# Optimization experiments

Hardware: AMD Instinct MI355X
Metric: run time of the kernel (lower is better)

## Reference

```python
import jax, jax.numpy as jnp
import numpy as np

IN_CH, HID, H1, H2, C2, OUT = 13, 64, 4, 2, 32, 1
NEG_SLOPE = 0.2  # PyG GATConv leaky_relu slope
BN_EPS = 1e-5


def _gat_layer(x, src, dst, N, W, att_src, att_dst, bias, heads, ch, concat):
    # x: [N, F_in]; W: [F_in, heads*ch]; att_*: [heads, ch]
    h = (x @ W).reshape(N, heads, ch)                      # [N,H,C]
    a_src = jnp.sum(h * att_src, axis=-1)                  # [N,H]
    a_dst = jnp.sum(h * att_dst, axis=-1)                  # [N,H]
    alpha = jax.nn.leaky_relu(a_src[src] + a_dst[dst], NEG_SLOPE)  # [E,H]
    # segment softmax over incoming edges of each dst node
    amax = jax.ops.segment_max(alpha, dst, num_segments=N)         # [N,H]
    e = jnp.exp(alpha - amax[dst])
    denom = jax.ops.segment_sum(e, dst, num_segments=N)
    alpha = e / denom[dst]                                 # [E,H]
    msg = h[src] * alpha[:, :, None]                       # [E,H,C]
    out = jax.ops.segment_sum(msg, dst, num_segments=N)    # [N,H,C]
    if concat:
        return out.reshape(N, heads * ch) + bias
    return out.mean(axis=1) + bias


def _with_self_loops(edge_index, N):
    loop = jnp.arange(N, dtype=edge_index.dtype)
    src = jnp.concatenate([edge_index[0], loop])
    dst = jnp.concatenate([edge_index[1], loop])
    return src, dst


def setup_inputs() -> dict:
    key = jax.random.key(0)
    ks = jax.random.split(key, 12)
    N, E = 50000, 800000
    glorot = lambda k, shp: jax.random.normal(k, shp, jnp.float32) * np.sqrt(2.0 / (shp[0] + shp[-1]))
    return {
        "x": jax.random.normal(ks[0], (N, IN_CH), jnp.float32),
        "edge_index": jax.random.randint(ks[1], (2, E), 0, N, dtype=jnp.int64 if jax.config.jax_enable_x64 else jnp.int32),
        "W1": glorot(ks[2], (IN_CH, H1 * HID)),
        "att_src1": glorot(ks[3], (H1, HID)),
        "att_dst1": glorot(ks[4], (H1, HID)),
        "b1": jnp.zeros((H1 * HID,), jnp.float32),
        "gamma1": jnp.ones((H1 * HID,), jnp.float32),
        "beta1": jnp.zeros((H1 * HID,), jnp.float32),
        "W2": glorot(ks[5], (H1 * HID, H2 * C2)),
        "att_src2": glorot(ks[6], (H2, C2)),
        "att_dst2": glorot(ks[7], (H2, C2)),
        "b2": jnp.zeros((C2,), jnp.float32),
        "Wc": glorot(ks[8], (C2, OUT)),
        "bc": jnp.zeros((OUT,), jnp.float32),
    }


def reference(x, edge_index, W1, att_src1, att_dst1, b1, gamma1, beta1,
              W2, att_src2, att_dst2, b2, Wc, bc):
    N = x.shape[0]
    src, dst = _with_self_loops(edge_index, N)  # PyG GATConv add_self_loops=True
    # layer 1: heads=4, concat=True -> [N, 256]
    h = _gat_layer(x, src, dst, N, W1, att_src1, att_dst1, b1, H1, HID, True)
    # BatchNorm1d (batch statistics) + ELU
    mu = h.mean(axis=0)
    var = h.var(axis=0)
    h = (h - mu) * jax.lax.rsqrt(var + BN_EPS) * gamma1 + beta1
    h = jax.nn.elu(h)
    # layer 2: heads=2, concat=False (mean over heads) -> [N, 32]
    h = _gat_layer(h, src, dst, N, W2, att_src2, att_dst2, b2, H2, C2, False)
    h = jax.nn.elu(h)
    return h @ Wc + bc  # [N, 1] logits
```

## Files before the change

### kernel.cpp

```cpp
#include <hip/hip_runtime.h>
#include <cstdint>
#include <cstddef>


#define NEG_SLOPE 0.2f
#define BN_EPS 1e-5f

__global__ __launch_bounds__(64) void kp_proj(
    const float* __restrict__ W1, const float* __restrict__ att_src1,
    const float* __restrict__ att_dst1, float* __restrict__ CS,
    float* __restrict__ CD) {
  int t = threadIdx.x;
  if (t >= 52) return;
  int k = t >> 2, h = t & 3;
  float cs = 0.f, cd = 0.f;
#pragma unroll 8
  for (int c = 0; c < 64; ++c) {
    float w = W1[k * 256 + h * 64 + c];
    cs = fmaf(w, att_src1[h * 64 + c], cs);
    cd = fmaf(w, att_dst1[h * 64 + c], cd);
  }
  CS[k * 4 + h] = cs;
  CD[k * 4 + h] = cd;
}

__global__ __launch_bounds__(256) void ka_logits(
    const float* __restrict__ x, const float* __restrict__ CS,
    const float* __restrict__ CD, float* __restrict__ as1,
    float* __restrict__ ad1, int N) {
  int n = blockIdx.x * blockDim.x + threadIdx.x;
  if (n >= N) return;
  float xr[13];
#pragma unroll
  for (int k = 0; k < 13; ++k) xr[k] = x[(size_t)n * 13 + k];
#pragma unroll
  for (int h = 0; h < 4; ++h) {
    float as = 0.f, ad = 0.f;
#pragma unroll
    for (int k = 0; k < 13; ++k) {
      as = fmaf(xr[k], CS[k * 4 + h], as);
      ad = fmaf(xr[k], CD[k * 4 + h], ad);
    }
    as1[(size_t)n * 4 + h] = as;
    ad1[(size_t)n * 4 + h] = ad;
  }
}

__global__ void kc_hist(const int* __restrict__ dst, int* __restrict__ curs,
                        int E, int Et) {
  int e = blockIdx.x * blockDim.x + threadIdx.x;
  if (e >= Et) return;
  int d = (e < E) ? dst[e] : (e - E);
  atomicAdd(&curs[d], 1);
}

__global__ __launch_bounds__(1024) void kc_scan1(
    const int* __restrict__ curs, int* __restrict__ rowptr,
    int* __restrict__ blocksum, int N) {
  __shared__ int sdata[1024];
  int t = threadIdx.x;
  int gid = blockIdx.x * 1024 + t;
  int v = (gid < N) ? curs[gid] : 0;
  sdata[t] = v;
  __syncthreads();
  for (int o = 1; o < 1024; o <<= 1) {
    int u = (t >= o) ? sdata[t - o] : 0;
    __syncthreads();
    sdata[t] += u;
    __syncthreads();
  }
  if (gid < N) rowptr[gid] = sdata[t] - v;
  if (t == 1023) blocksum[blockIdx.x] = sdata[1023];
}

__global__ __launch_bounds__(1024) void kc_scan2(int* __restrict__ blocksum,
                                                 int NB) {
  __shared__ int sd[1024];
  int t = threadIdx.x;
  int v = (t < NB) ? blocksum[t] : 0;
  sd[t] = v;
  __syncthreads();
  for (int o = 1; o < 1024; o <<= 1) {
    int u = (t >= o) ? sd[t - o] : 0;
    __syncthreads();
    sd[t] += u;
    __syncthreads();
  }
  if (t < NB) blocksum[t] = sd[t] - v;
}

__global__ __launch_bounds__(1024) void kc_scan3(
    int* __restrict__ rowptr, int* __restrict__ curs,
    const int* __restrict__ blocksum, int N, int Et) {
  int gid = blockIdx.x * 1024 + threadIdx.x;
  if (gid < N) {
    int val = rowptr[gid] + blocksum[blockIdx.x];
    rowptr[gid] = val;
    curs[gid] = val;
  }
  if (gid == 0) rowptr[N] = Et;
}

__global__ void kc_scatter(const int* __restrict__ src, const int* __restrict__ dst,
                           int* __restrict__ curs, int* __restrict__ csrs,
                           int E, int Et) {
  int e = blockIdx.x * blockDim.x + threadIdx.x;
  if (e >= Et) return;
  int s, d;
  if (e < E) { s = src[e]; d = dst[e]; } else { s = d = e - E; }
  int pos = atomicAdd(&curs[d], 1);
  csrs[pos] = s;
}

__global__ __launch_bounds__(256) void agg_x(
    const float* __restrict__ x, const float* __restrict__ as1,
    const float* __restrict__ ad1, const int* __restrict__ rowptr,
    const int* __restrict__ csrs, float* __restrict__ y, int N) {
  int wv = threadIdx.x >> 6, lane = threadIdx.x & 63;
  int d = blockIdx.x * 4 + wv;
  if (d >= N) return;
  int r0 = rowptr[d], r1 = rowptr[d + 1];
  float4 adv = *(const float4*)(ad1 + (size_t)d * 4);
  int hh = lane / 13;
  int kk = lane - hh * 13;
  float acc = 0.f;
  float s0 = 0.f, s1 = 0.f, s2 = 0.f, s3 = 0.f;
  for (int base = r0; base < r1; base += 64) {
    int cd = min(64, r1 - base);
    int s = 0;
    float e0 = 0.f, e1 = 0.f, e2 = 0.f, e3 = 0.f;
    if (lane < cd) {
      s = csrs[base + lane];
      float4 av = *(const float4*)(as1 + (size_t)s * 4);
      float l0 = av.x + adv.x; l0 = l0 >= 0.f ? l0 : NEG_SLOPE * l0;
      float l1 = av.y + adv.y; l1 = l1 >= 0.f ? l1 : NEG_SLOPE * l1;
      float l2 = av.z + adv.z; l2 = l2 >= 0.f ? l2 : NEG_SLOPE * l2;
      float l3 = av.w + adv.w; l3 = l3 >= 0.f ? l3 : NEG_SLOPE * l3;
      e0 = __expf(l0); e1 = __expf(l1); e2 = __expf(l2); e3 = __expf(l3);
      s0 += e0; s1 += e1; s2 += e2; s3 += e3;
    }
    for (int k = 0; k < cd; ++k) {
      int sk = __shfl(s, k);
      float w0 = __shfl(e0, k), w1 = __shfl(e1, k);
      float w2 = __shfl(e2, k), w3 = __shfl(e3, k);
      float w = hh == 0 ? w0 : hh == 1 ? w1 : hh == 2 ? w2 : w3;
      float xv = (lane < 52) ? x[(size_t)sk * 13 + kk] : 0.f;
      acc = fmaf(w, xv, acc);
    }
  }
#pragma unroll
  for (int m = 32; m; m >>= 1) {
    s0 += __shfl_xor(s0, m); s1 += __shfl_xor(s1, m);
    s2 += __shfl_xor(s2, m); s3 += __shfl_xor(s3, m);
  }
  if (lane < 52) {
    float den = hh == 0 ? s0 : hh == 1 ? s1 : hh == 2 ? s2 : s3;
    y[(size_t)d * 52 + lane] = acc / den;
  }
}

__global__ __launch_bounds__(256) void k1b_dense(
    const float* __restrict__ y, const float* __restrict__ W1,
    float* __restrict__ o1, float* __restrict__ bnsum,
    float* __restrict__ bnsq, int N) {
  __shared__ float W1s[13 * 256];
  int f = threadIdx.x;
  for (int idx = f; idx < 13 * 256; idx += 256) W1s[idx] = W1[idx];
  __syncthreads();
  int w = f >> 6, lane = f & 63;
  float s = 0.f, sq = 0.f;
  for (int n = blockIdx.x; n < N; n += gridDim.x) {
    float yv = (lane < 13) ? y[(size_t)n * 52 + w * 13 + lane] : 0.f;
    float acc = 0.f;
#pragma unroll
    for (int k = 0; k < 13; ++k)
      acc = fmaf(__shfl(yv, k), W1s[k * 256 + f], acc);
    o1[(size_t)n * 256 + f] = acc;
    s += acc;
    sq += acc * acc;
  }
  unsafeAtomicAdd(&bnsum[f], s);
  unsafeAtomicAdd(&bnsq[f], sq);
}

__global__ __launch_bounds__(256) void k6_bn_elu(
    float* __restrict__ o1, const float* __restrict__ bnsum,
    const float* __restrict__ bnsq, const float* __restrict__ gamma,
    const float* __restrict__ beta, int N) {
  size_t total = (size_t)N * 256;
  float invN = 1.0f / (float)N;
  for (size_t idx = (size_t)blockIdx.x * 256 + threadIdx.x; idx < total;
       idx += (size_t)gridDim.x * 256) {
    int f = (int)(idx & 255);
    float mu = bnsum[f] * invN;
    float var = bnsq[f] * invN - mu * mu;
    float v = (o1[idx] - mu) * rsqrtf(var + BN_EPS) * gamma[f] + beta[f];
    o1[idx] = v > 0.f ? v : expm1f(v);
  }
}

__global__ __launch_bounds__(256) void k7_linear2(
    const float* __restrict__ hbn, const float* __restrict__ W2,
    const float* __restrict__ att_src2, const float* __restrict__ att_dst2,
    float* __restrict__ h2, float* __restrict__ a_src2, float* __restrict__ a_dst2,
    int N) {
  __shared__ float rows[4][256];
  int wv = threadIdx.x >> 6, lane = threadIdx.x & 63;
  int n = blockIdx.x * 4 + wv;
  bool act = n < N;
  if (act) {
#pragma unroll
    for (int i = 0; i < 4; ++i)
      rows[wv][lane + i * 64] = hbn[(size_t)n * 256 + lane + i * 64];
  }
  __syncthreads();
  if (!act) return;
  float acc = 0.f;
#pragma unroll 8
  for (int k = 0; k < 256; ++k) acc = fmaf(rows[wv][k], W2[k * 64 + lane], acc);
  h2[(size_t)n * 64 + lane] = acc;
  int g = lane >> 5, c = lane & 31;
  float ps = acc * att_src2[g * 32 + c];
  float pd = acc * att_dst2[g * 32 + c];
#pragma unroll
  for (int m = 16; m; m >>= 1) {
    ps += __shfl_xor(ps, m);
    pd += __shfl_xor(pd, m);
  }
  if (c == 0) {
    a_src2[(size_t)n * 2 + g] = ps;
    a_dst2[(size_t)n * 2 + g] = pd;
  }
}

__global__ __launch_bounds__(256) void kagg2_head(
    const float* __restrict__ h2, const float* __restrict__ as2,
    const float* __restrict__ ad2, const int* __restrict__ rowptr,
    const int* __restrict__ csrs, const float* __restrict__ b2,
    const float* __restrict__ Wc, const float* __restrict__ bc,
    float* __restrict__ out, int N) {
  int wv = threadIdx.x >> 6, lane = threadIdx.x & 63;
  int d = blockIdx.x * 4 + wv;
  if (d >= N) return;
  int r0 = rowptr[d], r1 = rowptr[d + 1];
  float2 adv = *(const float2*)(ad2 + (size_t)d * 2);
  int head = lane >> 5;
  float fa = 0.f, s0 = 0.f, s1 = 0.f;
  for (int base = r0; base < r1; base += 64) {
    int cd = min(64, r1 - base);
    int s = 0;
    float e0 = 0.f, e1 = 0.f;
    if (lane < cd) {
      s = csrs[base + lane];
      float2 av = *(const float2*)(as2 + (size_t)s * 2);
      float l0 = av.x + adv.x; l0 = l0 >= 0.f ? l0 : NEG_SLOPE * l0;
      float l1 = av.y + adv.y; l1 = l1 >= 0.f ? l1 : NEG_SLOPE * l1;
      e0 = __expf(l0); e1 = __expf(l1);
      s0 += e0; s1 += e1;
    }
    for (int k = 0; k < cd; ++k) {
      int sk = __shfl(s, k);
      float w0 = __shfl(e0, k), w1 = __shfl(e1, k);
      float v = h2[(size_t)sk * 64 + lane];
      fa = fmaf(head ? w1 : w0, v, fa);
    }
  }
#pragma unroll
  for (int m = 32; m; m >>= 1) {
    s0 += __shfl_xor(s0, m);
    s1 += __shfl_xor(s1, m);
  }
  float o2v = fa / (head ? s1 : s0);
  float partner = __shfl_xor(o2v, 32);
  if (lane < 32) {
    float m = 0.5f * (o2v + partner) + b2[lane];
    m = m > 0.f ? m : expm1f(m);
    float t = m * Wc[lane];
#pragma unroll
    for (int mk = 16; mk; mk >>= 1) t += __shfl_xor(t, mk);
    if (lane == 0) out[d] = t + bc[0];
  }
}

extern "C" void kernel_launch(void* const* d_in, const int* in_sizes, int n_in,
                              void* d_out, int out_size, void* d_ws, size_t ws_size,
                              hipStream_t stream) {
  const float* x = (const float*)d_in[0];
  const int* ei = (const int*)d_in[1];
  const float* W1 = (const float*)d_in[2];
  const float* as1w = (const float*)d_in[3];
  const float* ad1w = (const float*)d_in[4];
  const float* gamma1 = (const float*)d_in[6];
  const float* beta1 = (const float*)d_in[7];
  const float* W2 = (const float*)d_in[8];
  const float* as2w = (const float*)d_in[9];
  const float* ad2w = (const float*)d_in[10];
  const float* b2 = (const float*)d_in[11];
  const float* Wc = (const float*)d_in[12];
  const float* bc = (const float*)d_in[13];

  const int N = in_sizes[0] / 13;
  const int E = in_sizes[1] / 2;
  const int Et = E + N;
  const int* srcp = ei;
  const int* dstp = ei + E;

  float* ws = (float*)d_ws;
  float* O1 = ws;
  float* Y = O1 + (size_t)N * 256;
  float* AS1 = Y + (size_t)N * 52;
  float* AD1 = AS1 + (size_t)N * 4;
  float* H2 = AD1 + (size_t)N * 4;
  float* AS2 = H2 + (size_t)N * 64;
  float* AD2 = AS2 + (size_t)N * 2;
  float* CS = AD2 + (size_t)N * 2;
  float* CD = CS + 64;
  float* BNS = CD + 64;
  float* BNQ = BNS + 256;
  int* ROWPTR = (int*)(BNQ + 256);
  int* CURS = ROWPTR + (N + 1);
  int* CSRS = CURS + N;
  int* BLKSUM = CSRS + Et;

  hipMemsetAsync(CURS, 0, (size_t)N * sizeof(int), stream);
  hipMemsetAsync(BNS, 0, 512 * sizeof(float), stream);

  int eb = (Et + 255) / 256;
  int nbs = (N + 1023) / 1024;
  kc_hist<<<eb, 256, 0, stream>>>(dstp, CURS, E, Et);
  kc_scan1<<<nbs, 1024, 0, stream>>>(CURS, ROWPTR, BLKSUM, N);
  kc_scan2<<<1, 1024, 0, stream>>>(BLKSUM, nbs);
  kc_scan3<<<nbs, 1024, 0, stream>>>(ROWPTR, CURS, BLKSUM, N, Et);
  kc_scatter<<<eb, 256, 0, stream>>>(srcp, dstp, CURS, CSRS, E, Et);

  kp_proj<<<1, 64, 0, stream>>>(W1, as1w, ad1w, CS, CD);
  ka_logits<<<(N + 255) / 256, 256, 0, stream>>>(x, CS, CD, AS1, AD1, N);
  agg_x<<<(N + 3) / 4, 256, 0, stream>>>(x, AS1, AD1, ROWPTR, CSRS, Y, N);
  k1b_dense<<<256, 256, 0, stream>>>(Y, W1, O1, BNS, BNQ, N);
  k6_bn_elu<<<4096, 256, 0, stream>>>(O1, BNS, BNQ, gamma1, beta1, N);

  k7_linear2<<<(N + 3) / 4, 256, 0, stream>>>(O1, W2, as2w, ad2w, H2, AS2, AD2, N);
  kagg2_head<<<(N + 3) / 4, 256, 0, stream>>>(H2, AS2, AD2, ROWPTR, CSRS,
                                              b2, Wc, bc, (float*)d_out, N);
}
```

Before: 520.9 us.

## Fuse BatchNorm+ELU into layer-2 GEMM with LDS-resident W2 and row tiling

```diff
diff --git a/kernel.cpp b/kernel.cpp
--- a/kernel.cpp
+++ b/kernel.cpp
@@ -183,53 +183,85 @@
   unsafeAtomicAdd(&bnsq[f], sq);
 }
 
-__global__ __launch_bounds__(256) void k6_bn_elu(
-    float* __restrict__ o1, const float* __restrict__ bnsum,
+__global__ __launch_bounds__(256) void k67_bn_gemm(
+    const float* __restrict__ o1raw, const float* __restrict__ bnsum,
     const float* __restrict__ bnsq, const float* __restrict__ gamma,
-    const float* __restrict__ beta, int N) {
-  size_t total = (size_t)N * 256;
-  float invN = 1.0f / (float)N;
-  for (size_t idx = (size_t)blockIdx.x * 256 + threadIdx.x; idx < total;
-       idx += (size_t)gridDim.x * 256) {
-    int f = (int)(idx & 255);
-    float mu = bnsum[f] * invN;
-    float var = bnsq[f] * invN - mu * mu;
-    float v = (o1[idx] - mu) * rsqrtf(var + BN_EPS) * gamma[f] + beta[f];
-    o1[idx] = v > 0.f ? v : expm1f(v);
-  }
-}
-
-__global__ __launch_bounds__(256) void k7_linear2(
-    const float* __restrict__ hbn, const float* __restrict__ W2,
+    const float* __restrict__ beta, const float* __restrict__ W2,
     const float* __restrict__ att_src2, const float* __restrict__ att_dst2,
-    float* __restrict__ h2, float* __restrict__ a_src2, float* __restrict__ a_dst2,
-    int N) {
-  __shared__ float rows[4][256];
-  int wv = threadIdx.x >> 6, lane = threadIdx.x & 63;
-  int n = blockIdx.x * 4 + wv;
-  bool act = n < N;
-  if (act) {
-#pragma unroll
-    for (int i = 0; i < 4; ++i)
-      rows[wv][lane + i * 64] = hbn[(size_t)n * 256 + lane + i * 64];
+    float* __restrict__ h2, float* __restrict__ a_src2,
+    float* __restrict__ a_dst2, int N, float invN) {
+  __shared__ float W2s[256 * 64];
+  __shared__ float sb[2][256];
+  __shared__ float rows[32][256];
+  int t = threadIdx.x;
+  for (int idx = t; idx < 256 * 64; idx += 256) W2s[idx] = W2[idx];
+  {
+    float mu = bnsum[t] * invN;
+    float var = bnsq[t] * invN - mu * mu;
+    float sc = rsqrtf(var + BN_EPS) * gamma[t];
+    sb[0][t] = sc;
+    sb[1][t] = beta[t] - mu * sc;
   }
   __syncthreads();
-  if (!act) return;
-  float acc = 0.f;
-#pragma unroll 8
-  for (int k = 0; k < 256; ++k) acc = fmaf(rows[wv][k], W2[k * 64 + lane], acc);
-  h2[(size_t)n * 64 + lane] = acc;
+  int wv = t >> 6, lane = t & 63;
   int g = lane >> 5, c = lane & 31;
-  float ps = acc * att_src2[g * 32 + c];
-  float pd = acc * att_dst2[g * 32 + c];
-#pragma unroll
-  for (int m = 16; m; m >>= 1) {
-    ps += __shfl_xor(ps, m);
-    pd += __shfl_xor(pd, m);
-  }
-  if (c == 0) {
-    a_src2[(size_t)n * 2 + g] = ps;
-    a_dst2[(size_t)n * 2 + g] = pd;
+  float asv = att_src2[lane];
+  float adv = att_dst2[lane];
+  for (int base = blockIdx.x * 32; base < N; base += gridDim.x * 32) {
+    for (int idx = t; idx < 32 * 256; idx += 256) {
+      int r = idx >> 8, f = idx & 255;
+      int n = base + r;
+      float v = 0.f;
+      if (n < N) {
+        v = fmaf(o1raw[(size_t)n * 256 + f], sb[0][f], sb[1][f]);
+        v = v > 0.f ? v : expm1f(v);
+      }
+      rows[r][f] = v;
+    }
+    __syncthreads();
+    const float* r0 = rows[8 * wv + 0];
+    const float* r1 = rows[8 * wv + 1];
+    const float* r2 = rows[8 * wv + 2];
+    const float* r3 = rows[8 * wv + 3];
+    const float* r4 = rows[8 * wv + 4];
+    const float* r5 = rows[8 * wv + 5];
+    const float* r6 = rows[8 * wv + 6];
+    const float* r7 = rows[8 * wv + 7];
+    float a0 = 0.f, a1 = 0.f, a2 = 0.f, a3 = 0.f;
+    float a4 = 0.f, a5 = 0.f, a6 = 0.f, a7 = 0.f;
+#pragma unroll 4
+    for (int k = 0; k < 256; ++k) {
+      float w2v = W2s[k * 64 + lane];
+      a0 = fmaf(r0[k], w2v, a0);
+      a1 = fmaf(r1[k], w2v, a1);
+      a2 = fmaf(r2[k], w2v, a2);
+      a3 = fmaf(r3[k], w2v, a3);
+      a4 = fmaf(r4[k], w2v, a4);
+      a5 = fmaf(r5[k], w2v, a5);
+      a6 = fmaf(r6[k], w2v, a6);
+      a7 = fmaf(r7[k], w2v, a7);
+    }
+#pragma unroll
+    for (int r = 0; r < 8; ++r) {
+      float acc = r == 0 ? a0 : r == 1 ? a1 : r == 2 ? a2 : r == 3 ? a3
+                : r == 4 ? a4 : r == 5 ? a5 : r == 6 ? a6 : a7;
+      int n = base + 8 * wv + r;
+      if (n < N) {
+        h2[(size_t)n * 64 + lane] = acc;
+        float ps = acc * asv;
+        float pd = acc * adv;
+#pragma unroll
+        for (int m = 16; m; m >>= 1) {
+          ps += __shfl_xor(ps, m);
+          pd += __shfl_xor(pd, m);
+        }
+        if (c == 0) {
+          a_src2[(size_t)n * 2 + g] = ps;
+          a_dst2[(size_t)n * 2 + g] = pd;
+        }
+      }
+    }
+    __syncthreads();
   }
 }
 
@@ -337,9 +369,10 @@
   ka_logits<<<(N + 255) / 256, 256, 0, stream>>>(x, CS, CD, AS1, AD1, N);
   agg_x<<<(N + 3) / 4, 256, 0, stream>>>(x, AS1, AD1, ROWPTR, CSRS, Y, N);
   k1b_dense<<<256, 256, 0, stream>>>(Y, W1, O1, BNS, BNQ, N);
-  k6_bn_elu<<<4096, 256, 0, stream>>>(O1, BNS, BNQ, gamma1, beta1, N);
-
-  k7_linear2<<<(N + 3) / 4, 256, 0, stream>>>(O1, W2, as2w, ad2w, H2, AS2, AD2, N);
+
+  k67_bn_gemm<<<256, 256, 0, stream>>>(O1, BNS, BNQ, gamma1, beta1, W2,
+                                       as2w, ad2w, H2, AS2, AD2, N,
+                                       1.0f / (float)N);
   kagg2_head<<<(N + 3) / 4, 256, 0, stream>>>(H2, AS2, AD2, ROWPTR, CSRS,
                                               b2, Wc, bc, (float*)d_out, N);
 }
```

After: 582.1 us. 11.8% more time.
